# Kernel tuning notes

Measured on AMD Instinct MI355X. Metric: run time of the kernel, lower is better.

The kernel has to match this reference:

```python
import jax, jax.numpy as jnp
import numpy as np

NUM_EMBEDDINGS = 1024
EMBEDDING_DIM = 256


def setup_inputs() -> dict:
    key = jax.random.key(0)
    k1, k2 = jax.random.split(key)
    z = jax.random.normal(k1, (32, EMBEDDING_DIM, 32, 32), dtype=jnp.float32)
    codebook = jax.random.normal(k2, (NUM_EMBEDDINGS, EMBEDDING_DIM), dtype=jnp.float32)
    return {"z": z, "codebook": codebook}


def reference(z, codebook):
    # z: (B, C, H, W) -> (B, H, W, C) -> (B*H*W, C)
    B, C, H, W = z.shape
    z_bhwc = jnp.transpose(z, (0, 2, 3, 1))
    z_flat = z_bhwc.reshape(-1, C)  # (N, C)

    # pairwise squared distances: ||z||^2 + ||e||^2 - 2 z.e^T  -> (N, K)
    distances = (
        jnp.sum(z_flat ** 2, axis=1, keepdims=True)
        + jnp.sum(codebook ** 2, axis=1)
        - 2.0 * jnp.matmul(z_flat, codebook.T)
    )
    argmin_codewords = jnp.argmin(distances, axis=1)  # (N,)
    min_codewords = jax.nn.one_hot(argmin_codewords, NUM_EMBEDDINGS, dtype=jnp.float32)  # (N, K)

    # quantized latents via one-hot @ codebook, back to (B, C, H, W)
    z_quantized = jnp.matmul(min_codewords, codebook).reshape(B, H, W, C)
    z_quantized = jnp.transpose(z_quantized, (0, 3, 1, 2))
    return (min_codewords, z_quantized)
```

## Files before the change

### kernel.cpp

```cpp
#include <hip/hip_runtime.h>

#define N_ROWS 32768
#define K_CODES 1024
#define CDIM 256

typedef _Float16 half8 __attribute__((ext_vector_type(8)));
typedef _Float16 half4 __attribute__((ext_vector_type(4)));
typedef float floatx16 __attribute__((ext_vector_type(16)));
typedef unsigned long long ull;

#define WS_ZH   0ull
#define WS_ZL   16777216ull
#define WS_CBH  33554432ull
#define WS_CBL  34078720ull
#define WS_CBN  34603008ull
#define WS_PART 34607104ull
#define WS_IDX  36704256ull
#define WS_NEED 36835328ull

__device__ __forceinline__ void g2lds16(const void* g, void* l) {
    __builtin_amdgcn_global_load_lds(
        (const __attribute__((address_space(1))) void*)g,
        (__attribute__((address_space(3))) void*)l, 16, 0, 0);
}

#define WAITCNT_VM4() __builtin_amdgcn_s_waitcnt(4 | (7 << 4) | (15 << 8))
#define WAITCNT_VM0() __builtin_amdgcn_s_waitcnt(0 | (7 << 4) | (15 << 8))


__global__ __launch_bounds__(64) void cb_prep(const float* __restrict__ cb,
                                              _Float16* __restrict__ cbh,
                                              _Float16* __restrict__ cbl,
                                              float* __restrict__ cbn) {
    int k = blockIdx.x;
    int lane = threadIdx.x;
    float4 v = reinterpret_cast<const float4*>(cb + k * CDIM)[lane];
    float s0 = v.x * 32.f, s1 = v.y * 32.f, s2 = v.z * 32.f, s3 = v.w * 32.f;
    half4 hv, lv;
    hv[0] = (_Float16)s0; lv[0] = (_Float16)(s0 - (float)hv[0]);
    hv[1] = (_Float16)s1; lv[1] = (_Float16)(s1 - (float)hv[1]);
    hv[2] = (_Float16)s2; lv[2] = (_Float16)(s2 - (float)hv[2]);
    hv[3] = (_Float16)s3; lv[3] = (_Float16)(s3 - (float)hv[3]);
    int ccq = lane >> 1;
    size_t off = (size_t)(ccq * K_CODES + k) * 8 + (lane & 1) * 4;
    *reinterpret_cast<half4*>(&cbh[off]) = hv;
    *reinterpret_cast<half4*>(&cbl[off]) = lv;
    float s = s0 * s0 + s1 * s1 + s2 * s2 + s3 * s3;
    #pragma unroll
    for (int off2 = 32; off2 > 0; off2 >>= 1) s += __shfl_down(s, off2);
    if (lane == 0) cbn[k] = s;
}

__global__ __launch_bounds__(256) void z_prep(const float* __restrict__ z,
                                              _Float16* __restrict__ zh,
                                              _Float16* __restrict__ zl) {
    __shared__ float t[64][68];
    int hwt = blockIdx.x & 15;
    int ct  = (blockIdx.x >> 4) & 3;
    int bb  = blockIdx.x >> 6;
    int tid = threadIdx.x;
    #pragma unroll
    for (int p = 0; p < 4; p++) {
        int e = p * 256 + tid;
        int c = e >> 4, h4 = e & 15;
        float4 v = *reinterpret_cast<const float4*>(
            &z[((bb * 256 + ct * 64 + c) << 10) + hwt * 64 + h4 * 4]);
        *reinterpret_cast<float4*>(&t[c][h4 * 4]) = v;
    }
    __syncthreads();
    int hw = tid & 63, g8 = tid >> 6;
    int n = bb * 1024 + hwt * 64 + hw;
    #pragma unroll
    for (int p = 0; p < 2; p++) {
        int o = g8 * 2 + p;
        int ccq = (ct * 64 + o * 8) >> 3;
        half8 hv, lv;
        #pragma unroll
        for (int j = 0; j < 8; j++) {
            float s = t[o * 8 + j][hw] * 32.f;
            _Float16 h = (_Float16)s;
            hv[j] = h;
            lv[j] = (_Float16)(s - (float)h);
        }
        size_t off = (size_t)(ccq * N_ROWS + n) * 8;
        *reinterpret_cast<half8*>(&zh[off]) = hv;
        *reinterpret_cast<half8*>(&zl[off]) = lv;
    }
}

__global__ __launch_bounds__(256, 3) void vq_pipe(
    const _Float16* __restrict__ zh, const _Float16* __restrict__ zl,
    const _Float16* __restrict__ cbh, const _Float16* __restrict__ cbl,
    const float* __restrict__ cbn, ull* __restrict__ partial) {

    __shared__ _Float16 AhL[3][2048], AlL[3][2048];
    __shared__ _Float16 BhL[3][2048], BlL[3][2048];

    const int tid = threadIdx.x;
    const int lane = tid & 63, wave = tid >> 6;
    const int wm = wave & 1, wn = wave >> 1;
    const int fm = lane & 31, fq = lane >> 5;
    const int codeTile = blockIdx.x >> 8;
    const int g = blockIdx.x & 255;
    const int rowTile = (g & 7) * 32 + (g >> 3);
    const int rowBase = rowTile * 128, codeBase = codeTile * 128;

    const int sq = tid >> 7, sr = tid & 127;
    const size_t aBase = (size_t)(rowBase + sr) * 8;
    const size_t bBase = (size_t)(codeBase + sr) * 8;

    floatx16 acc[4];
    #pragma unroll
    for (int i = 0; i < 4; i++) acc[i] = (floatx16)0.f;

    {
        size_t soA = (size_t)(sq * N_ROWS) * 8 + aBase;
        size_t soB = (size_t)(sq * K_CODES) * 8 + bBase;
        int d = (sq * 128 + sr) * 8;
        g2lds16(zh + soA,  &AhL[0][d]);
        g2lds16(zl + soA,  &AlL[0][d]);
        g2lds16(cbh + soB, &BhL[0][d]);
        g2lds16(cbl + soB, &BlL[0][d]);
    }

    #pragma unroll
    for (int k = 0; k < 16; k++) {
        const int cbuf = k % 3;
        if (k < 15) {
            const int nbuf = (k + 1) % 3;
            const int ccq = 2 * (k + 1) + sq;
            size_t soA = (size_t)(ccq * N_ROWS) * 8 + aBase;
            size_t soB = (size_t)(ccq * K_CODES) * 8 + bBase;
            int d = (sq * 128 + sr) * 8;
            g2lds16(zh + soA,  &AhL[nbuf][d]);
            g2lds16(zl + soA,  &AlL[nbuf][d]);
            g2lds16(cbh + soB, &BhL[nbuf][d]);
            g2lds16(cbl + soB, &BlL[nbuf][d]);
            WAITCNT_VM4();
        } else {
            WAITCNT_VM0();
        }
        __builtin_amdgcn_s_barrier();

        half8 ah[2], al[2], bh[2], bl[2];
        #pragma unroll
        for (int i = 0; i < 2; i++) {
            int ga = (fq * 128 + wm * 64 + i * 32 + fm) * 8;
            ah[i] = *reinterpret_cast<const half8*>(&AhL[cbuf][ga]);
            al[i] = *reinterpret_cast<const half8*>(&AlL[cbuf][ga]);
        }
        #pragma unroll
        for (int j = 0; j < 2; j++) {
            int gb = (fq * 128 + wn * 64 + j * 32 + fm) * 8;
            bh[j] = *reinterpret_cast<const half8*>(&BhL[cbuf][gb]);
            bl[j] = *reinterpret_cast<const half8*>(&BlL[cbuf][gb]);
        }
        #pragma unroll
        for (int i = 0; i < 2; i++)
            #pragma unroll
            for (int j = 0; j < 2; j++) {
                acc[i*2+j] = __builtin_amdgcn_mfma_f32_32x32x16_f16(ah[i], bh[j], acc[i*2+j], 0, 0, 0);
                acc[i*2+j] = __builtin_amdgcn_mfma_f32_32x32x16_f16(al[i], bh[j], acc[i*2+j], 0, 0, 0);
                acc[i*2+j] = __builtin_amdgcn_mfma_f32_32x32x16_f16(ah[i], bl[j], acc[i*2+j], 0, 0, 0);
            }
    }
    __syncthreads();

    float (*rvv)[2] = reinterpret_cast<float(*)[2]>(&AhL[0][0]);
    int   (*rcc)[2] = reinterpret_cast<int(*)[2]>(&AhL[0][1024]);

    float cbnv[2];
    #pragma unroll
    for (int j = 0; j < 2; j++) cbnv[j] = cbn[codeBase + wn * 64 + j * 32 + fm];

    #pragma unroll
    for (int i = 0; i < 2; i++)
        #pragma unroll
        for (int r = 0; r < 16; r++) {
            float best = 3.4e38f; int bcode = 0x7fffffff;
            #pragma unroll
            for (int j = 0; j < 2; j++) {
                float d = fmaf(-2.f, acc[i*2+j][r], cbnv[j]);
                int code = codeBase + wn * 64 + j * 32 + fm;
                if (d < best) { best = d; bcode = code; }
            }
            #pragma unroll
            for (int m = 1; m < 32; m <<= 1) {
                float ov = __shfl_xor(best, m, 64);
                int   oc = __shfl_xor(bcode, m, 64);
                if (ov < best || (ov == best && oc < bcode)) { best = ov; bcode = oc; }
            }
            if (fm == 0) {
                int row = wm * 64 + i * 32 + (r & 3) + 8 * (r >> 2) + 4 * fq;
                rvv[row][wn] = best;
                rcc[row][wn] = bcode;
            }
        }
    __syncthreads();
    if (tid < 128) {
        float v0 = rvv[tid][0]; int c0 = rcc[tid][0];
        float v1 = rvv[tid][1]; int c1 = rcc[tid][1];
        if (v1 < v0 || (v1 == v0 && c1 < c0)) { v0 = v1; c0 = c1; }
        unsigned u = __float_as_uint(v0);
        u = (u & 0x80000000u) ? ~u : (u | 0x80000000u);
        partial[(size_t)(rowBase + tid) * 8 + codeTile] =
            ((ull)u << 32) | (unsigned)c0;
    }
}

__global__ __launch_bounds__(256) void onehot_fin(const ull* __restrict__ partial,
                                                  int* __restrict__ idx,
                                                  float* __restrict__ out) {
    int row = blockIdx.x;
    __shared__ int sid;
    if (threadIdx.x < 64) {
        ull v = (threadIdx.x < 8) ? partial[(size_t)row * 8 + threadIdx.x]
                                  : ~0ull;
        #pragma unroll
        for (int m = 1; m < 8; m <<= 1) {
            ull o = __shfl_xor(v, m, 64);
            if (o < v) v = o;
        }
        if (threadIdx.x == 0) {
            int id = (int)(v & 0xffffffffu);
            sid = id;
            idx[row] = id;
        }
    }
    __syncthreads();
    int id = sid;
    int k4 = threadIdx.x << 2;
    float4 v4;
    v4.x = (k4     == id) ? 1.f : 0.f;
    v4.y = (k4 + 1 == id) ? 1.f : 0.f;
    v4.z = (k4 + 2 == id) ? 1.f : 0.f;
    v4.w = (k4 + 3 == id) ? 1.f : 0.f;
    reinterpret_cast<float4*>(out)[(size_t)row * 256 + threadIdx.x] = v4;
}

__global__ __launch_bounds__(256) void zq_fill(const int* __restrict__ idx,
                                               const float* __restrict__ cb,
                                               float* __restrict__ out) {
    int i  = blockIdx.x * 256 + threadIdx.x;
    int hw = i & 1023;
    int c  = (i >> 10) & 255;
    int b  = i >> 18;
    int n  = (b << 10) | hw;
    out[i] = cb[idx[n] * CDIM + c];
}


__global__ __launch_bounds__(64) void cb_norms(const float* __restrict__ cb,
                                               float* __restrict__ cbn) {
    int k = blockIdx.x;
    int lane = threadIdx.x;
    float4 v = reinterpret_cast<const float4*>(cb + k * CDIM)[lane];
    float s = v.x * v.x + v.y * v.y + v.z * v.z + v.w * v.w;
    #pragma unroll
    for (int off = 32; off > 0; off >>= 1) s += __shfl_down(s, off);
    if (lane == 0) cbn[k] = s;
}

__global__ __launch_bounds__(256) void cb_transpose(const float* __restrict__ cb,
                                                    float* __restrict__ cbt) {
    __shared__ float t[32][33];
    int k0 = (blockIdx.x & 31) * 32;
    int c0 = (blockIdx.x >> 5) * 32;
    int lane = threadIdx.x & 31;
    int row = threadIdx.x >> 5;
    #pragma unroll
    for (int s = 0; s < 4; s++) {
        int r = row + s * 8;
        t[r][lane] = cb[(k0 + r) * CDIM + c0 + lane];
    }
    __syncthreads();
    #pragma unroll
    for (int s = 0; s < 4; s++) {
        int r = row + s * 8;
        cbt[(c0 + r) * K_CODES + k0 + lane] = t[lane][r];
    }
}

__global__ __launch_bounds__(512, 2) void vq_argmin(const float* __restrict__ z,
                                                    const float* __restrict__ cbt,
                                                    const float* __restrict__ cbn,
                                                    int* __restrict__ idx_out) {
    __shared__ float As[64][128];
    __shared__ float Bs[64][256];

    const int tid = threadIdx.x;
    const int tx = tid & 31;
    const int ty = tid >> 5;
    const int rowBase = blockIdx.x * 128;
    const int bb = rowBase >> 10;
    const int hwBase = rowBase & 1023;

    float minv[8];
    int   mini[8];
    #pragma unroll
    for (int i = 0; i < 8; i++) { minv[i] = 3.4e38f; mini[i] = 0; }

    for (int kt = 0; kt < K_CODES; kt += 256) {
        float acc[2][2][4][4];
        #pragma unroll
        for (int a = 0; a < 2; a++)
            #pragma unroll
            for (int b = 0; b < 2; b++)
                #pragma unroll
                for (int i = 0; i < 4; i++)
                    #pragma unroll
                    for (int j = 0; j < 4; j++) acc[a][b][i][j] = 0.f;

        for (int ccb = 0; ccb < CDIM; ccb += 64) {
            #pragma unroll
            for (int l = 0; l < 4; l++) {
                int f = tid + l * 512;
                int r4 = f & 31, c = f >> 5;
                float4 v = *reinterpret_cast<const float4*>(
                    &z[((bb * 256 + ccb + c) << 10) + hwBase + r4 * 4]);
                *reinterpret_cast<float4*>(&As[c][r4 * 4]) = v;
            }
            #pragma unroll
            for (int l = 0; l < 8; l++) {
                int f = tid + l * 512;
                int k4 = f & 63, c = f >> 6;
                float4 v = *reinterpret_cast<const float4*>(
                    &cbt[(ccb + c) * K_CODES + kt + k4 * 4]);
                *reinterpret_cast<float4*>(&Bs[c][k4 * 4]) = v;
            }
            __syncthreads();
            #pragma unroll 4
            for (int c = 0; c < 64; c++) {
                float4 a0 = *reinterpret_cast<const float4*>(&As[c][ty * 4]);
                float4 a1 = *reinterpret_cast<const float4*>(&As[c][64 + ty * 4]);
                float4 b0 = *reinterpret_cast<const float4*>(&Bs[c][tx * 4]);
                float4 b1 = *reinterpret_cast<const float4*>(&Bs[c][128 + tx * 4]);
                float av[2][4] = {{a0.x, a0.y, a0.z, a0.w}, {a1.x, a1.y, a1.z, a1.w}};
                float bw[2][4] = {{b0.x, b0.y, b0.z, b0.w}, {b1.x, b1.y, b1.z, b1.w}};
                #pragma unroll
                for (int ri = 0; ri < 2; ri++)
                    #pragma unroll
                    for (int i = 0; i < 4; i++)
                        #pragma unroll
                        for (int ci = 0; ci < 2; ci++)
                            #pragma unroll
                            for (int j = 0; j < 4; j++)
                                acc[ri][ci][i][j] =
                                    fmaf(av[ri][i], bw[ci][j], acc[ri][ci][i][j]);
            }
            __syncthreads();
        }
        #pragma unroll
        for (int ci = 0; ci < 2; ci++)
            #pragma unroll
            for (int j = 0; j < 4; j++) {
                int code = kt + ci * 128 + tx * 4 + j;
                float nrm = cbn[code];
                #pragma unroll
                for (int ri = 0; ri < 2; ri++)
                    #pragma unroll
                    for (int i = 0; i < 4; i++) {
                        float d = fmaf(-2.f, acc[ri][ci][i][j], nrm);
                        int r = ri * 4 + i;
                        if (d < minv[r]) { minv[r] = d; mini[r] = code; }
                    }
            }
    }

    __syncthreads();
    float (*rv)[32] = reinterpret_cast<float(*)[32]>(&As[0][0]);
    int   (*rix)[32] = reinterpret_cast<int(*)[32]>(&As[32][0]);
    #pragma unroll
    for (int ri = 0; ri < 2; ri++)
        #pragma unroll
        for (int i = 0; i < 4; i++) {
            int row = ri * 64 + ty * 4 + i;
            rv[row][tx] = minv[ri * 4 + i];
            rix[row][tx] = mini[ri * 4 + i];
        }
    __syncthreads();
    if (tid < 128) {
        float bvv = rv[tid][0]; int bii = rix[tid][0];
        #pragma unroll
        for (int t = 1; t < 32; t++) {
            float v = rv[tid][t]; int ii = rix[tid][t];
            if (v < bvv || (v == bvv && ii < bii)) { bvv = v; bii = ii; }
        }
        idx_out[rowBase + tid] = bii;
    }
}

__global__ __launch_bounds__(256) void onehot_fill(const int* __restrict__ idx,
                                                   float* __restrict__ out) {
    int i = blockIdx.x * 256 + threadIdx.x;
    int n  = i >> 8;
    int k4 = (i & 255) << 2;
    int id = idx[n];
    float4 v;
    v.x = (k4     == id) ? 1.f : 0.f;
    v.y = (k4 + 1 == id) ? 1.f : 0.f;
    v.z = (k4 + 2 == id) ? 1.f : 0.f;
    v.w = (k4 + 3 == id) ? 1.f : 0.f;
    reinterpret_cast<float4*>(out)[i] = v;
}

extern "C" void kernel_launch(void* const* d_in, const int* in_sizes, int n_in,
                              void* d_out, int out_size, void* d_ws, size_t ws_size,
                              hipStream_t stream) {
    const float* z  = (const float*)d_in[0];
    const float* cb = (const float*)d_in[1];
    float* out0 = (float*)d_out;
    float* out1 = out0 + (size_t)N_ROWS * K_CODES;

    if (ws_size >= WS_NEED) {
        _Float16* zh  = (_Float16*)((char*)d_ws + WS_ZH);
        _Float16* zl  = (_Float16*)((char*)d_ws + WS_ZL);
        _Float16* cbh = (_Float16*)((char*)d_ws + WS_CBH);
        _Float16* cbl = (_Float16*)((char*)d_ws + WS_CBL);
        float* cbn = (float*)((char*)d_ws + WS_CBN);
        ull* part = (ull*)((char*)d_ws + WS_PART);
        int* idx = (int*)((char*)d_ws + WS_IDX);

        cb_prep<<<K_CODES, 64, 0, stream>>>(cb, cbh, cbl, cbn);
        z_prep<<<2048, 256, 0, stream>>>(z, zh, zl);
        vq_pipe<<<2048, 256, 0, stream>>>(zh, zl, cbh, cbl, cbn, part);
        onehot_fin<<<N_ROWS, 256, 0, stream>>>(part, idx, out0);
        zq_fill<<<(N_ROWS * CDIM) / 256, 256, 0, stream>>>(idx, cb, out1);
    } else {
        float* cbn = (float*)d_ws;
        int*   idx = (int*)((char*)d_ws + 4096);
        float* cbt = (float*)((char*)d_ws + 4096 + 131072);

        cb_norms<<<K_CODES, 64, 0, stream>>>(cb, cbn);
        cb_transpose<<<256, 256, 0, stream>>>(cb, cbt);
        vq_argmin<<<N_ROWS / 128, 512, 0, stream>>>(z, cbt, cbn, idx);
        onehot_fill<<<(N_ROWS * K_CODES / 4) / 256, 256, 0, stream>>>(idx, out0);
        zq_fill<<<(N_ROWS * CDIM) / 256, 256, 0, stream>>>(idx, cb, out1);
    }
}
```

Before: 315.2 us.

## Load GEMM fragments directly from global memory instead of LDS pipeline

```diff
diff --git a/kernel.cpp b/kernel.cpp
--- a/kernel.cpp
+++ b/kernel.cpp
@@ -17,15 +17,6 @@
 #define WS_PART 34607104ull
 #define WS_IDX  36704256ull
 #define WS_NEED 36835328ull
-
-__device__ __forceinline__ void g2lds16(const void* g, void* l) {
-    __builtin_amdgcn_global_load_lds(
-        (const __attribute__((address_space(1))) void*)g,
-        (__attribute__((address_space(3))) void*)l, 16, 0, 0);
-}
-
-#define WAITCNT_VM4() __builtin_amdgcn_s_waitcnt(4 | (7 << 4) | (15 << 8))
-#define WAITCNT_VM0() __builtin_amdgcn_s_waitcnt(0 | (7 << 4) | (15 << 8))
 
 
 __global__ __launch_bounds__(64) void cb_prep(const float* __restrict__ cb,
@@ -88,13 +79,13 @@
     }
 }
 
-__global__ __launch_bounds__(256, 3) void vq_pipe(
+__global__ __launch_bounds__(256, 3) void vq_direct(
     const _Float16* __restrict__ zh, const _Float16* __restrict__ zl,
     const _Float16* __restrict__ cbh, const _Float16* __restrict__ cbl,
     const float* __restrict__ cbn, ull* __restrict__ partial) {
 
-    __shared__ _Float16 AhL[3][2048], AlL[3][2048];
-    __shared__ _Float16 BhL[3][2048], BlL[3][2048];
+    __shared__ float rvv[128][2];
+    __shared__ int   rcc[128][2];
 
     const int tid = threadIdx.x;
     const int lane = tid & 63, wave = tid >> 6;
@@ -105,55 +96,27 @@
     const int rowTile = (g & 7) * 32 + (g >> 3);
     const int rowBase = rowTile * 128, codeBase = codeTile * 128;
 
-    const int sq = tid >> 7, sr = tid & 127;
-    const size_t aBase = (size_t)(rowBase + sr) * 8;
-    const size_t bBase = (size_t)(codeBase + sr) * 8;
+    const size_t aBase = ((size_t)fq * N_ROWS + rowBase + wm * 64 + fm) * 8;
+    const size_t bBase = ((size_t)fq * K_CODES + codeBase + wn * 64 + fm) * 8;
 
     floatx16 acc[4];
     #pragma unroll
     for (int i = 0; i < 4; i++) acc[i] = (floatx16)0.f;
 
-    {
-        size_t soA = (size_t)(sq * N_ROWS) * 8 + aBase;
-        size_t soB = (size_t)(sq * K_CODES) * 8 + bBase;
-        int d = (sq * 128 + sr) * 8;
-        g2lds16(zh + soA,  &AhL[0][d]);
-        g2lds16(zl + soA,  &AlL[0][d]);
-        g2lds16(cbh + soB, &BhL[0][d]);
-        g2lds16(cbl + soB, &BlL[0][d]);
-    }
-
     #pragma unroll
     for (int k = 0; k < 16; k++) {
-        const int cbuf = k % 3;
-        if (k < 15) {
-            const int nbuf = (k + 1) % 3;
-            const int ccq = 2 * (k + 1) + sq;
-            size_t soA = (size_t)(ccq * N_ROWS) * 8 + aBase;
-            size_t soB = (size_t)(ccq * K_CODES) * 8 + bBase;
-            int d = (sq * 128 + sr) * 8;
-            g2lds16(zh + soA,  &AhL[nbuf][d]);
-            g2lds16(zl + soA,  &AlL[nbuf][d]);
-            g2lds16(cbh + soB, &BhL[nbuf][d]);
-            g2lds16(cbl + soB, &BlL[nbuf][d]);
-            WAITCNT_VM4();
-        } else {
-            WAITCNT_VM0();
-        }
-        __builtin_amdgcn_s_barrier();
-
+        const size_t ao = aBase + (size_t)(2 * k) * N_ROWS * 8;
+        const size_t bo = bBase + (size_t)(2 * k) * K_CODES * 8;
         half8 ah[2], al[2], bh[2], bl[2];
         #pragma unroll
         for (int i = 0; i < 2; i++) {
-            int ga = (fq * 128 + wm * 64 + i * 32 + fm) * 8;
-            ah[i] = *reinterpret_cast<const half8*>(&AhL[cbuf][ga]);
-            al[i] = *reinterpret_cast<const half8*>(&AlL[cbuf][ga]);
+            ah[i] = *reinterpret_cast<const half8*>(zh + ao + i * 32 * 8);
+            al[i] = *reinterpret_cast<const half8*>(zl + ao + i * 32 * 8);
         }
         #pragma unroll
         for (int j = 0; j < 2; j++) {
-            int gb = (fq * 128 + wn * 64 + j * 32 + fm) * 8;
-            bh[j] = *reinterpret_cast<const half8*>(&BhL[cbuf][gb]);
-            bl[j] = *reinterpret_cast<const half8*>(&BlL[cbuf][gb]);
+            bh[j] = *reinterpret_cast<const half8*>(cbh + bo + j * 32 * 8);
+            bl[j] = *reinterpret_cast<const half8*>(cbl + bo + j * 32 * 8);
         }
         #pragma unroll
         for (int i = 0; i < 2; i++)
@@ -164,10 +127,6 @@
                 acc[i*2+j] = __builtin_amdgcn_mfma_f32_32x32x16_f16(ah[i], bl[j], acc[i*2+j], 0, 0, 0);
             }
     }
-    __syncthreads();
-
-    float (*rvv)[2] = reinterpret_cast<float(*)[2]>(&AhL[0][0]);
-    int   (*rcc)[2] = reinterpret_cast<int(*)[2]>(&AhL[0][1024]);
 
     float cbnv[2];
     #pragma unroll
@@ -423,7 +382,7 @@
 
         cb_prep<<<K_CODES, 64, 0, stream>>>(cb, cbh, cbl, cbn);
         z_prep<<<2048, 256, 0, stream>>>(z, zh, zl);
-        vq_pipe<<<2048, 256, 0, stream>>>(zh, zl, cbh, cbl, cbn, part);
+        vq_direct<<<2048, 256, 0, stream>>>(zh, zl, cbh, cbl, cbn, part);
         onehot_fin<<<N_ROWS, 256, 0, stream>>>(part, idx, out0);
         zq_fill<<<(N_ROWS * CDIM) / 256, 256, 0, stream>>>(idx, cb, out1);
     } else {
```

New measurement: 307.4 us. 2.5% less time.
